# Kernel optimization log

Hardware: AMD Instinct MI355X
Metric: run time of the kernel (lower is better)

The kernel has to match this reference:

```python
import jax, jax.numpy as jnp
import numpy as np

# Config (from Mamba3Config defaults)
D_MODEL = 768
EXPAND = 4
D_INNER = EXPAND * D_MODEL          # 3072
D_HEAD = 64
N_HEADS = D_INNER // D_HEAD         # 48
N_EXPERTS = 8
TOP_K = 2
R3 = 256                            # latent MoE input dim
R2 = 1024                           # latent MoE output dim
EPS = 1e-5
TANH_SCALE = 10.0                   # fast_scaled_tanh default
ROUTER_TEMP = 0.5                   # get_router_temperature(step=None) -> t_end


def _rms_norm(x, w):
    return x * jax.lax.rsqrt(jnp.mean(x * x, axis=-1, keepdims=True) + EPS) * w


def _scaled_tanh(x):
    return TANH_SCALE * jnp.tanh(x * (1.0 / TANH_SCALE))


def setup_inputs() -> dict:
    key = jax.random.key(0)
    ks = jax.random.split(key, 13)
    s = 0.02
    B, L = 2, 4096
    return {
        "x": jax.random.normal(ks[0], (B, L, D_MODEL), dtype=jnp.float32),
        "rms1_w": jnp.ones((D_MODEL,), jnp.float32),
        "W_in": s * jax.random.normal(ks[1], (D_MODEL, 2 * D_INNER + N_HEADS), jnp.float32),
        "dt_bias": jax.random.uniform(ks[2], (N_HEADS,), jnp.float32, -4.0, -1.0),  # dt in [dt_min, dt_max]-ish
        "W_out": s * jax.random.normal(ks[3], (D_INNER, D_MODEL), jnp.float32),
        "ls1": 0.01 * jnp.ones((D_MODEL,), jnp.float32),
        "rms2_w": jnp.ones((D_MODEL,), jnp.float32),
        "W_down": s * jax.random.normal(ks[4], (D_MODEL, R3), jnp.float32),
        "W_router": s * jax.random.normal(ks[5], (D_MODEL, N_EXPERTS), jnp.float32),
        "G": s * jax.random.normal(ks[6], (N_EXPERTS, R3, R2), jnp.float32),
        "W_up": s * jax.random.normal(ks[7], (R2, D_MODEL), jnp.float32),
        "ls2": 0.01 * jnp.ones((D_MODEL,), jnp.float32),
    }


def reference(x, rms1_w, W_in, dt_bias, W_out, ls1, rms2_w, W_down, W_router, G, W_up, ls2):
    B, L, _ = x.shape
    # ---- Mamba selective-scan branch ----
    xn = _rms_norm(x, rms1_w)
    proj = xn @ W_in                                   # [B,L,2*Di+H]
    u, z, dt = jnp.split(proj, [D_INNER, 2 * D_INNER], axis=-1)
    log_alpha = -jax.nn.softplus(dt + dt_bias)         # [B,L,H], per-head scalar decay
    alpha = jnp.exp(log_alpha)[..., None]              # [B,L,H,1]
    u4 = u.reshape(B, L, N_HEADS, D_HEAD)

    def combine(left, right):                          # first_order_combine_op
        a_l, b_l = left
        a_r, b_r = right
        return (a_r * a_l, a_r * b_l + b_r)

    _, h = jax.lax.associative_scan(
        combine, (jnp.broadcast_to(alpha, u4.shape), u4), axis=1)
    y = h.reshape(B, L, D_INNER) * jax.nn.silu(z)
    y = _scaled_tanh(y)
    x1 = x + ls1 * (y @ W_out)

    # ---- Fused latent MoE (Tucker) branch ----
    x2n = _rms_norm(x1, rms2_w)
    lat = _scaled_tanh(x2n @ W_down)                   # [B,L,r3]
    logits = (x2n @ W_router) * (1.0 / ROUTER_TEMP)    # [B,L,E]
    vals, idx = jax.lax.top_k(logits, TOP_K)
    probs = jax.nn.softmax(vals, axis=-1)              # [B,L,K]
    # dense combine weights: w[b,l,e] = sum_k probs_k * [idx_k == e]
    w = jnp.sum(jax.nn.one_hot(idx, N_EXPERTS, dtype=lat.dtype) * probs[..., None], axis=-2)
    # out[b,l,c] = sum_e w[b,l,e] * (lat[b,l,:] @ G[e])  (== fused gather grouped-GEMM)
    moe = jnp.einsum('blr,erc,ble->blc', lat, G, w)    # [B,L,r2]
    out = x1 + ls2 * (moe @ W_up)
    return out
```

## Files before the change

kernel.cpp:

```cpp
#include <hip/hip_runtime.h>
#include <stdint.h>

typedef unsigned short ushort_t;
typedef __attribute__((ext_vector_type(8))) __bf16 bf16x8;
typedef __attribute__((ext_vector_type(4))) float floatx4;
typedef __attribute__((ext_vector_type(4))) unsigned short ushort4v;
typedef __attribute__((ext_vector_type(8))) unsigned short ushort8v;

#define TT 8192L
#define LB 4096L
#define DD 768L
#define DI 3072L
#define NH 48L
#define R3C 256L
#define R2C 1024L
#define NP 6272L
#define NCH 64L
#define CHS 64L

__device__ __forceinline__ float b2f(ushort_t u) {
  union { unsigned u32; float f; } v; v.u32 = ((unsigned)u) << 16; return v.f;
}
__device__ __forceinline__ ushort_t f2b(float f) {
  union { float f; unsigned u32; } v; v.f = f;
  unsigned r = v.u32 + 0x7FFFu + ((v.u32 >> 16) & 1u);
  return (ushort_t)(r >> 16);
}
__device__ __forceinline__ float fast_tanh(float x) {
  float e = __expf(2.0f * x);
  return 1.0f - 2.0f / (e + 1.0f);
}
__device__ __forceinline__ void g2l16(const void* g, void* l) {
  __builtin_amdgcn_global_load_lds(
      (const __attribute__((address_space(1))) unsigned int*)g,
      (__attribute__((address_space(3))) unsigned int*)l, 16, 0, 0);
}

__global__ __launch_bounds__(256) void k_tr(const float* __restrict__ src,
                                            ushort_t* __restrict__ dst,
                                            int K, int N) {
  __shared__ float tile[64][65];
  int k0 = blockIdx.x * 64, n0 = blockIdx.y * 64;
  int c = threadIdx.x & 63, r4 = threadIdx.x >> 6;
#pragma unroll
  for (int s = 0; s < 16; s++) {
    int r = s * 4 + r4;
    int n = n0 + c;
    tile[c][r] = (n < N) ? src[(long)(k0 + r) * N + n] : 0.0f;
  }
  __syncthreads();
#pragma unroll
  for (int s = 0; s < 16; s++) {
    int r = s * 4 + r4;
    dst[(long)(n0 + r) * K + k0 + c] = f2b(tile[r][c]);
  }
}

__global__ __launch_bounds__(256) void k_rms(const float* __restrict__ x,
                                             const float* __restrict__ w,
                                             ushort_t* __restrict__ out) {
  int t = blockIdx.x, tid = threadIdx.x;
  int lane = tid & 63, wid = tid >> 6;
  const float* xr = x + (long)t * DD;
  float v0 = xr[tid], v1 = xr[tid + 256], v2 = xr[tid + 512];
  float ss = v0 * v0 + v1 * v1 + v2 * v2;
  for (int o = 32; o; o >>= 1) ss += __shfl_down(ss, o);
  __shared__ float red[4];
  if (lane == 0) red[wid] = ss;
  __syncthreads();
  float tot = red[0] + red[1] + red[2] + red[3];
  float rr = rsqrtf(tot / 768.0f + 1e-5f);
  ushort_t* orow = out + (long)t * DD;
  orow[tid]       = f2b(v0 * rr * w[tid]);
  orow[tid + 256] = f2b(v1 * rr * w[tid + 256]);
  orow[tid + 512] = f2b(v2 * rr * w[tid + 512]);
}

__global__ __launch_bounds__(256) void k_rms2_router(const ushort_t* __restrict__ x1,
                                                     const float* __restrict__ w,
                                                     const float* __restrict__ wr,
                                                     ushort_t* __restrict__ x2n,
                                                     float* __restrict__ wrt) {
  int t = blockIdx.x, tid = threadIdx.x;
  int lane = tid & 63, wid = tid >> 6;
  const ushort_t* xr = x1 + (long)t * DD;
  float v[3];
  int dd[3] = {tid, tid + 256, tid + 512};
  v[0] = b2f(xr[dd[0]]); v[1] = b2f(xr[dd[1]]); v[2] = b2f(xr[dd[2]]);
  float ss = v[0] * v[0] + v[1] * v[1] + v[2] * v[2];
  for (int o = 32; o; o >>= 1) ss += __shfl_down(ss, o);
  __shared__ float red[4];
  __shared__ float wred[4][8];
  __shared__ float slog[8];
  if (lane == 0) red[wid] = ss;
  __syncthreads();
  float tot = red[0] + red[1] + red[2] + red[3];
  float rr = rsqrtf(tot / 768.0f + 1e-5f);
  float p[8] = {0, 0, 0, 0, 0, 0, 0, 0};
  ushort_t* orow = x2n + (long)t * DD;
#pragma unroll
  for (int i = 0; i < 3; i++) {
    float xnv = v[i] * rr * w[dd[i]];
    orow[dd[i]] = f2b(xnv);
    const float* wrow = wr + (long)dd[i] * 8;
#pragma unroll
    for (int e = 0; e < 8; e++) p[e] += xnv * wrow[e];
  }
#pragma unroll
  for (int e = 0; e < 8; e++) {
    float s = p[e];
    for (int o = 32; o; o >>= 1) s += __shfl_down(s, o);
    if (lane == 0) wred[wid][e] = s;
  }
  __syncthreads();
  if (tid < 8)
    slog[tid] = (wred[0][tid] + wred[1][tid] + wred[2][tid] + wred[3][tid]) * 2.0f;
  __syncthreads();
  if (tid == 0) {
    float l[8];
#pragma unroll
    for (int e = 0; e < 8; e++) l[e] = slog[e];
    int e0 = 0; float b0 = l[0];
#pragma unroll
    for (int e = 1; e < 8; e++) if (l[e] > b0) { b0 = l[e]; e0 = e; }
    int e1 = -1; float b1 = -1e30f;
#pragma unroll
    for (int e = 0; e < 8; e++) if (e != e0 && l[e] > b1) { b1 = l[e]; e1 = e; }
    float ex = __expf(b1 - b0);
    float pd = 1.0f / (1.0f + ex);
    float* wo = wrt + (long)t * 8;
#pragma unroll
    for (int e = 0; e < 8; e++) wo[e] = 0.0f;
    wo[e0] = pd;
    wo[e1] = ex * pd;
  }
}

__global__ __launch_bounds__(256) void k_alpha(const ushort_t* __restrict__ proj,
                                               const float* __restrict__ dtb,
                                               float* __restrict__ alpha) {
  int gid = blockIdx.x * 256 + threadIdx.x;
  int tg = gid / 48;
  int h = gid - tg * 48;
  float dt = b2f(proj[(long)tg * NP + 2 * DI + h]) + dtb[h];
  float sp = (dt > 20.0f) ? dt : log1pf(__expf(dt));
  alpha[(long)h * LB + tg] = __expf(-sp);
}

__device__ __forceinline__ void stage_tile(const ushort_t* __restrict__ g, long rowstride,
                                           ushort_t* __restrict__ lds, int lane) {
  const int lrow = lane >> 3;
  const int dcol = (lane & 7) * 8;
#pragma unroll
  for (int c8 = 0; c8 < 8; c8++) {
    ushort8v v = *(const ushort8v*)(g + (long)(c8 * 8 + lrow) * rowstride + dcol);
    *(ushort8v*)&lds[(c8 * 64 + lane) * 8] = v;
  }
}

__global__ __launch_bounds__(64) void k_scan1(const ushort_t* __restrict__ proj,
                                              const float* __restrict__ alpha,
                                              float* __restrict__ ssum,
                                              float* __restrict__ asum) {
  __shared__ __align__(16) ushort_t u_lds[64 * 64];
  __shared__ float s_alpha[64];
  const int lane = threadIdx.x;
  const int idx = blockIdx.x;
  const int c = idx & 63;
  const int h = idx >> 6;
  s_alpha[lane] = alpha[(long)h * LB + (long)c * CHS + lane];
  const ushort_t* ug = proj + (long)c * CHS * NP + (long)h * 64;
  stage_tile(ug, NP, u_lds, lane);
  __syncthreads();
  float s = 0.0f, A = 1.0f;
#pragma unroll
  for (int tt = 0; tt < 64; tt++) {
    float a = s_alpha[tt];
    float u = b2f(u_lds[tt * 64 + lane]);
    s = fmaf(a, s, u);
    A *= a;
  }
  ssum[(long)idx * 64 + lane] = s;
  if (lane == 0) asum[idx] = A;
}

__global__ __launch_bounds__(64) void k_scan2(const float* __restrict__ ssum,
                                              const float* __restrict__ asum,
                                              float* __restrict__ carry) {
  int h = blockIdx.x, lane = threadIdx.x;
  float cv = 0.0f;
  for (int c = 0; c < 64; c++) {
    carry[((long)h * 64 + c) * 64 + lane] = cv;
    float A = asum[h * 64 + c];
    float s = ssum[((long)h * 64 + c) * 64 + lane];
    cv = A * cv + s;
  }
}

__global__ __launch_bounds__(64) void k_scan3(const ushort_t* __restrict__ proj,
                                              const float* __restrict__ alpha,
                                              const float* __restrict__ carry,
                                              ushort_t* __restrict__ y) {
  __shared__ __align__(16) ushort_t u_lds[64 * 64];
  __shared__ __align__(16) ushort_t z_lds[64 * 64];
  __shared__ float s_alpha[64];
  const int lane = threadIdx.x;
  const int idx = blockIdx.x;
  const int c = idx & 63;
  const int h = idx >> 6;
  s_alpha[lane] = alpha[(long)h * LB + (long)c * CHS + lane];
  const ushort_t* ug = proj + (long)c * CHS * NP + (long)h * 64;
  const ushort_t* zg = ug + DI;
  ushort_t* yg = y + (long)c * CHS * DI + (long)h * 64;
  stage_tile(ug, NP, u_lds, lane);
  stage_tile(zg, NP, z_lds, lane);
  __syncthreads();
  float hs = carry[(long)idx * 64 + lane];
#pragma unroll
  for (int tt = 0; tt < 64; tt++) {
    float a = s_alpha[tt];
    float u = b2f(u_lds[tt * 64 + lane]);
    hs = fmaf(a, hs, u);
    float zv = b2f(z_lds[tt * 64 + lane]);
    float sig = 1.0f / (1.0f + __expf(-zv));
    float yv = hs * zv * sig;
    yv = 10.0f * fast_tanh(yv * 0.1f);
    yg[(long)tt * DI + lane] = f2b(yv);
  }
}

__global__ __launch_bounds__(256) void k_abig(const ushort_t* __restrict__ lat,
                                              const float* __restrict__ wrt,
                                              ushort_t* __restrict__ abig) {
  long gid = (long)blockIdx.x * 256 + threadIdx.x;
  long idx = gid * 4;
  int t = (int)(idx >> 11);
  int off = (int)(idx & 2047);
  int e = off >> 8, r = off & 255;
  float wv = wrt[(long)t * 8 + e];
  ushort4v lv = *(const ushort4v*)(lat + (long)t * R3C + r);
  ushort4v ov;
  ov.x = f2b(wv * b2f(lv.x));
  ov.y = f2b(wv * b2f(lv.y));
  ov.z = f2b(wv * b2f(lv.z));
  ov.w = f2b(wv * b2f(lv.w));
  *(ushort4v*)(abig + (long)t * 2048 + off) = ov;
}

template <int MODE>
__global__ __launch_bounds__(256, 2) void k_gemm(const ushort_t* __restrict__ A,
                                                 const ushort_t* __restrict__ Bt,
                                                 void* __restrict__ Cout, int K, int ldc,
                                                 const float* __restrict__ resf,
                                                 const ushort_t* __restrict__ resb,
                                                 const float* __restrict__ ls) {
  __shared__ __align__(16) ushort_t sA[128 * 32];
  __shared__ __align__(16) ushort_t sB[128 * 32];
  const int tid = threadIdx.x;
  const int lane = tid & 63, wid = tid >> 6;
  const int lm = lane & 15, q = lane >> 4;
  const int wm = wid >> 1, wn = wid & 1;
  const long row0 = (long)blockIdx.x * 128;
  const long col0 = (long)blockIdx.y * 128;

  floatx4 acc[4][4] = {};

  const int srow = wid * 32 + (lane >> 2);
  const int skoff = (lane & 3) * 8;
  const ushort_t* Ag0 = A + (row0 + srow) * (long)K + skoff;
  const ushort_t* Ag1 = Ag0 + 16L * K;
  const ushort_t* Bg0 = Bt + (col0 + srow) * (long)K + skoff;
  const ushort_t* Bg1 = Bg0 + 16L * K;
  ushort_t* sA0 = sA + wid * 1024;
  ushort_t* sB0 = sB + wid * 1024;

  for (int k0 = 0; k0 < K; k0 += 32) {
    g2l16(Ag0 + k0, sA0);
    g2l16(Ag1 + k0, sA0 + 512);
    g2l16(Bg0 + k0, sB0);
    g2l16(Bg1 + k0, sB0 + 512);
    __syncthreads();
    bf16x8 af[4], bfr[4];
#pragma unroll
    for (int i = 0; i < 4; i++)
      af[i] = *(const bf16x8*)(const void*)&sA[(wm * 64 + i * 16 + lm) * 32 + q * 8];
#pragma unroll
    for (int j = 0; j < 4; j++)
      bfr[j] = *(const bf16x8*)(const void*)&sB[(wn * 64 + j * 16 + lm) * 32 + q * 8];
#pragma unroll
    for (int i = 0; i < 4; i++)
#pragma unroll
      for (int j = 0; j < 4; j++)
        acc[i][j] = __builtin_amdgcn_mfma_f32_16x16x32_bf16(af[i], bfr[j], acc[i][j], 0, 0, 0);
    __syncthreads();
  }
#pragma unroll
  for (int i = 0; i < 4; i++) {
#pragma unroll
    for (int r = 0; r < 4; r++) {
      long row = row0 + wm * 64 + i * 16 + q * 4 + r;
#pragma unroll
      for (int j = 0; j < 4; j++) {
        long col = col0 + wn * 64 + j * 16 + lm;
        float v = acc[i][j][r];
        if (MODE == 0) {
          ((ushort_t*)Cout)[row * (long)ldc + col] = f2b(v);
        } else if (MODE == 2) {
          ((ushort_t*)Cout)[row * (long)ldc + col] = f2b(10.0f * fast_tanh(v * 0.1f));
        } else if (MODE == 1) {
          float rv = resf[row * DD + col];
          ((ushort_t*)Cout)[row * (long)ldc + col] = f2b(rv + ls[col] * v);
        } else {
          float rv = b2f(resb[row * DD + col]);
          ((float*)Cout)[row * (long)ldc + col] = rv + ls[col] * v;
        }
      }
    }
  }
}

#define OFF_WINT   0L
#define OFF_WOUTT  9633792L
#define OFF_WDNT   14352384L
#define OFF_WUPT   14745600L
#define OFF_GT     16318464L
#define OFF_X1     20512768L
#define OFF_WRT    33095680L
#define OFF_ALPHA  33357824L
#define OFF_SSUM   34144256L
#define OFF_ASUM   34930688L
#define OFF_CARRY  34942976L
#define OFF_XN     35729408L
#define OFF_Y      48312320L
#define OFF_PROJ   73478144L
#define OFF_ABIG   OFF_PROJ
#define OFF_LAT    (OFF_PROJ + 33554432L)
#define OFF_X2N    OFF_XN
#define OFF_MOE    OFF_Y
#define WS_NEEDED  124858368L

extern "C" void kernel_launch(void* const* d_in, const int* in_sizes, int n_in,
                              void* d_out, int out_size, void* d_ws, size_t ws_size,
                              hipStream_t stream) {
  const float* x     = (const float*)d_in[0];
  const float* rms1w = (const float*)d_in[1];
  const float* W_in  = (const float*)d_in[2];
  const float* dtb   = (const float*)d_in[3];
  const float* W_out = (const float*)d_in[4];
  const float* ls1   = (const float*)d_in[5];
  const float* rms2w = (const float*)d_in[6];
  const float* W_dn  = (const float*)d_in[7];
  const float* W_rtr = (const float*)d_in[8];
  const float* G     = (const float*)d_in[9];
  const float* W_up  = (const float*)d_in[10];
  const float* ls2   = (const float*)d_in[11];
  if (ws_size < (size_t)WS_NEEDED) return;

  char* ws = (char*)d_ws;
  ushort_t* W_inT  = (ushort_t*)(ws + OFF_WINT);
  ushort_t* W_outT = (ushort_t*)(ws + OFF_WOUTT);
  ushort_t* W_dnT  = (ushort_t*)(ws + OFF_WDNT);
  ushort_t* W_upT  = (ushort_t*)(ws + OFF_WUPT);
  ushort_t* GT     = (ushort_t*)(ws + OFF_GT);
  ushort_t* x1     = (ushort_t*)(ws + OFF_X1);
  float*    wrt    = (float*)(ws + OFF_WRT);
  float*    alpha  = (float*)(ws + OFF_ALPHA);
  float*    ssum   = (float*)(ws + OFF_SSUM);
  float*    asum   = (float*)(ws + OFF_ASUM);
  float*    carry  = (float*)(ws + OFF_CARRY);
  ushort_t* xn     = (ushort_t*)(ws + OFF_XN);
  ushort_t* y      = (ushort_t*)(ws + OFF_Y);
  ushort_t* proj   = (ushort_t*)(ws + OFF_PROJ);
  ushort_t* abig   = (ushort_t*)(ws + OFF_ABIG);
  ushort_t* lat    = (ushort_t*)(ws + OFF_LAT);
  ushort_t* x2n    = (ushort_t*)(ws + OFF_X2N);
  ushort_t* moe    = (ushort_t*)(ws + OFF_MOE);
  float*    outp   = (float*)d_out;

  k_tr<<<dim3(12, 98), 256, 0, stream>>>(W_in, W_inT, 768, 6192);
  k_tr<<<dim3(48, 12), 256, 0, stream>>>(W_out, W_outT, 3072, 768);
  k_tr<<<dim3(12, 4), 256, 0, stream>>>(W_dn, W_dnT, 768, 256);
  k_tr<<<dim3(16, 12), 256, 0, stream>>>(W_up, W_upT, 1024, 768);
  k_tr<<<dim3(32, 16), 256, 0, stream>>>(G, GT, 2048, 1024);

  k_rms<<<8192, 256, 0, stream>>>(x, rms1w, xn);

  for (int b = 0; b < 2; b++) {
    const ushort_t* xnb = xn + (long)b * LB * DD;
    k_gemm<0><<<dim3(32, 49), 256, 0, stream>>>(xnb, W_inT, proj, 768, (int)NP,
                                                nullptr, nullptr, nullptr);
    k_alpha<<<768, 256, 0, stream>>>(proj, dtb, alpha);
    k_scan1<<<3072, 64, 0, stream>>>(proj, alpha, ssum, asum);
    k_scan2<<<48, 64, 0, stream>>>(ssum, asum, carry);
    k_scan3<<<3072, 64, 0, stream>>>(proj, alpha, carry, y);
    k_gemm<1><<<dim3(32, 6), 256, 0, stream>>>(y, W_outT, x1 + (long)b * LB * DD, 3072, 768,
                                               x + (long)b * LB * DD, nullptr, ls1);
  }

  k_rms2_router<<<8192, 256, 0, stream>>>(x1, rms2w, W_rtr, x2n, wrt);
  k_gemm<2><<<dim3(64, 2), 256, 0, stream>>>(x2n, W_dnT, lat, 768, 256,
                                             nullptr, nullptr, nullptr);
  k_abig<<<16384, 256, 0, stream>>>(lat, wrt, abig);
  k_gemm<0><<<dim3(64, 8), 256, 0, stream>>>(abig, GT, moe, 2048, 1024,
                                             nullptr, nullptr, nullptr);
  k_gemm<3><<<dim3(64, 6), 256, 0, stream>>>(moe, W_upT, outp, 1024, 768,
                                             nullptr, x1, ls2);
}
```

Measured before the change: 605.2 us.

## Add split-K to small-grid GEMMs with separate reduction/epilogue kernels

The narrow GEMMs (W_out projection, W_down latent, W_up output) now split their K dimension across blockIdx.z and write fp32 partial sums to a workspace. Dedicated combine kernels then sum the partials and apply the residual/layer-scale or scaled-tanh epilogues. Launch bounds are raised to 4 blocks per SM. The aim is to fill more CUs for GEMMs whose grids were only 128–384 blocks. The cost is extra fp32 partial-buffer traffic and additional kernel launches.

```diff
diff --git a/kernel.cpp b/kernel.cpp
--- a/kernel.cpp
+++ b/kernel.cpp
@@ -15,7 +15,6 @@
 #define R3C 256L
 #define R2C 1024L
 #define NP 6272L
-#define NCH 64L
 #define CHS 64L
 
 __device__ __forceinline__ float b2f(ushort_t u) {
@@ -248,12 +247,10 @@
 }
 
 template <int MODE>
-__global__ __launch_bounds__(256, 2) void k_gemm(const ushort_t* __restrict__ A,
+__global__ __launch_bounds__(256, 4) void k_gemm(const ushort_t* __restrict__ A,
                                                  const ushort_t* __restrict__ Bt,
-                                                 void* __restrict__ Cout, int K, int ldc,
-                                                 const float* __restrict__ resf,
-                                                 const ushort_t* __restrict__ resb,
-                                                 const float* __restrict__ ls) {
+                                                 void* __restrict__ Cout, int K, int kstride,
+                                                 int ldc, long zoff) {
   __shared__ __align__(16) ushort_t sA[128 * 32];
   __shared__ __align__(16) ushort_t sB[128 * 32];
   const int tid = threadIdx.x;
@@ -262,15 +259,18 @@
   const int wm = wid >> 1, wn = wid & 1;
   const long row0 = (long)blockIdx.x * 128;
   const long col0 = (long)blockIdx.y * 128;
+  const int z = blockIdx.z;
+  A += (long)z * K;
+  Bt += (long)z * K;
 
   floatx4 acc[4][4] = {};
 
   const int srow = wid * 32 + (lane >> 2);
   const int skoff = (lane & 3) * 8;
-  const ushort_t* Ag0 = A + (row0 + srow) * (long)K + skoff;
-  const ushort_t* Ag1 = Ag0 + 16L * K;
-  const ushort_t* Bg0 = Bt + (col0 + srow) * (long)K + skoff;
-  const ushort_t* Bg1 = Bg0 + 16L * K;
+  const ushort_t* Ag0 = A + (row0 + srow) * (long)kstride + skoff;
+  const ushort_t* Ag1 = Ag0 + 16L * kstride;
+  const ushort_t* Bg0 = Bt + (col0 + srow) * (long)kstride + skoff;
+  const ushort_t* Bg1 = Bg0 + 16L * kstride;
   ushort_t* sA0 = sA + wid * 1024;
   ushort_t* sB0 = sB + wid * 1024;
 
@@ -305,18 +305,57 @@
         float v = acc[i][j][r];
         if (MODE == 0) {
           ((ushort_t*)Cout)[row * (long)ldc + col] = f2b(v);
-        } else if (MODE == 2) {
-          ((ushort_t*)Cout)[row * (long)ldc + col] = f2b(10.0f * fast_tanh(v * 0.1f));
-        } else if (MODE == 1) {
-          float rv = resf[row * DD + col];
-          ((ushort_t*)Cout)[row * (long)ldc + col] = f2b(rv + ls[col] * v);
         } else {
-          float rv = b2f(resb[row * DD + col]);
-          ((float*)Cout)[row * (long)ldc + col] = rv + ls[col] * v;
+          ((float*)Cout)[(long)z * zoff + row * (long)ldc + col] = v;
         }
       }
     }
   }
+}
+
+__global__ __launch_bounds__(256) void k_comb_res(const float* __restrict__ P, long zoff, int nz,
+                                                  const float* __restrict__ x,
+                                                  const float* __restrict__ ls,
+                                                  ushort_t* __restrict__ x1) {
+  long i = ((long)blockIdx.x * 256 + threadIdx.x) * 4;
+  float s[4] = {0, 0, 0, 0};
+  for (int zz = 0; zz < nz; zz++) {
+    const float* p = P + (long)zz * zoff + i;
+#pragma unroll
+    for (int j = 0; j < 4; j++) s[j] += p[j];
+  }
+  int c = (int)(i % DD);
+#pragma unroll
+  for (int j = 0; j < 4; j++) x1[i + j] = f2b(x[i + j] + ls[c + j] * s[j]);
+}
+
+__global__ __launch_bounds__(256) void k_comb_tanh(const float* __restrict__ P, long zoff, int nz,
+                                                   ushort_t* __restrict__ lat) {
+  long i = ((long)blockIdx.x * 256 + threadIdx.x) * 4;
+  float s[4] = {0, 0, 0, 0};
+  for (int zz = 0; zz < nz; zz++) {
+    const float* p = P + (long)zz * zoff + i;
+#pragma unroll
+    for (int j = 0; j < 4; j++) s[j] += p[j];
+  }
+#pragma unroll
+  for (int j = 0; j < 4; j++) lat[i + j] = f2b(10.0f * fast_tanh(0.1f * s[j]));
+}
+
+__global__ __launch_bounds__(256) void k_comb_out(const float* __restrict__ P, long zoff, int nz,
+                                                  const ushort_t* __restrict__ x1,
+                                                  const float* __restrict__ ls,
+                                                  float* __restrict__ outp) {
+  long i = ((long)blockIdx.x * 256 + threadIdx.x) * 4;
+  float s[4] = {0, 0, 0, 0};
+  for (int zz = 0; zz < nz; zz++) {
+    const float* p = P + (long)zz * zoff + i;
+#pragma unroll
+    for (int j = 0; j < 4; j++) s[j] += p[j];
+  }
+  int c = (int)(i % DD);
+#pragma unroll
+  for (int j = 0; j < 4; j++) outp[i + j] = b2f(x1[i + j]) + ls[c + j] * s[j];
 }
 
 #define OFF_WINT   0L
@@ -335,6 +374,7 @@
 #define OFF_PROJ   73478144L
 #define OFF_ABIG   OFF_PROJ
 #define OFF_LAT    (OFF_PROJ + 33554432L)
+#define OFF_PART   OFF_PROJ
 #define OFF_X2N    OFF_XN
 #define OFF_MOE    OFF_Y
 #define WS_NEEDED  124858368L
@@ -373,6 +413,7 @@
   ushort_t* proj   = (ushort_t*)(ws + OFF_PROJ);
   ushort_t* abig   = (ushort_t*)(ws + OFF_ABIG);
   ushort_t* lat    = (ushort_t*)(ws + OFF_LAT);
+  float*    part   = (float*)(ws + OFF_PART);
   ushort_t* x2n    = (ushort_t*)(ws + OFF_X2N);
   ushort_t* moe    = (ushort_t*)(ws + OFF_MOE);
   float*    outp   = (float*)d_out;
@@ -387,22 +428,21 @@
 
   for (int b = 0; b < 2; b++) {
     const ushort_t* xnb = xn + (long)b * LB * DD;
-    k_gemm<0><<<dim3(32, 49), 256, 0, stream>>>(xnb, W_inT, proj, 768, (int)NP,
-                                                nullptr, nullptr, nullptr);
+    k_gemm<0><<<dim3(32, 49, 1), 256, 0, stream>>>(xnb, W_inT, proj, 768, 768, (int)NP, 0);
     k_alpha<<<768, 256, 0, stream>>>(proj, dtb, alpha);
     k_scan1<<<3072, 64, 0, stream>>>(proj, alpha, ssum, asum);
     k_scan2<<<48, 64, 0, stream>>>(ssum, asum, carry);
     k_scan3<<<3072, 64, 0, stream>>>(proj, alpha, carry, y);
-    k_gemm<1><<<dim3(32, 6), 256, 0, stream>>>(y, W_outT, x1 + (long)b * LB * DD, 3072, 768,
-                                               x + (long)b * LB * DD, nullptr, ls1);
+    k_gemm<4><<<dim3(32, 6, 4), 256, 0, stream>>>(y, W_outT, part, 768, 3072, 768, LB * DD);
+    k_comb_res<<<3072, 256, 0, stream>>>(part, LB * DD, 4, x + (long)b * LB * DD, ls1,
+                                         x1 + (long)b * LB * DD);
   }
 
   k_rms2_router<<<8192, 256, 0, stream>>>(x1, rms2w, W_rtr, x2n, wrt);
-  k_gemm<2><<<dim3(64, 2), 256, 0, stream>>>(x2n, W_dnT, lat, 768, 256,
-                                             nullptr, nullptr, nullptr);
+  k_gemm<4><<<dim3(64, 2, 3), 256, 0, stream>>>(x2n, W_dnT, part, 256, 768, 256, TT * R3C);
+  k_comb_tanh<<<2048, 256, 0, stream>>>(part, TT * R3C, 3, lat);
   k_abig<<<16384, 256, 0, stream>>>(lat, wrt, abig);
-  k_gemm<0><<<dim3(64, 8), 256, 0, stream>>>(abig, GT, moe, 2048, 1024,
-                                             nullptr, nullptr, nullptr);
-  k_gemm<3><<<dim3(64, 6), 256, 0, stream>>>(moe, W_upT, outp, 1024, 768,
-                                             nullptr, x1, ls2);
-}
+  k_gemm<0><<<dim3(64, 8, 1), 256, 0, stream>>>(abig, GT, moe, 2048, 2048, 1024, 0);
+  k_gemm<4><<<dim3(64, 6, 2), 256, 0, stream>>>(moe, W_upT, part, 512, 1024, 768, TT * DD);
+  k_comb_out<<<6144, 256, 0, stream>>>(part, TT * DD, 2, x1, ls2, outp);
+}
```

Result: faster. 575.8 us (-4.9%).
